# Kernel optimization log

Hardware: AMD Instinct MI355X
Metric: run time of the kernel (lower is better)

## Reference

```python
import jax, jax.numpy as jnp
import numpy as np

B, L, D_MODEL = 4, 2048, 1024
D_INNER, D_STATE, D_CONV = 2 * D_MODEL, 16, 4
DT_RANK = (D_MODEL + 15) // 16  # 64


def silu(v):
    return v * jax.nn.sigmoid(v)


def setup_inputs() -> dict:
    key = jax.random.key(0)
    ks = jax.random.split(key, 8)
    n = lambda k, shape, s: jax.random.normal(k, shape, jnp.float32) * s
    A = jnp.broadcast_to(jnp.arange(1, D_STATE + 1, dtype=jnp.float32), (D_INNER, D_STATE))
    return {
        "x": jax.random.normal(ks[0], (B, L, D_MODEL), jnp.float32),
        "in_proj_w": n(ks[1], (2 * D_INNER, D_MODEL), 0.02),
        "conv_w": n(ks[2], (D_INNER, 1, D_CONV), 0.1),
        "conv_b": jnp.zeros((D_INNER,), jnp.float32),
        "x_proj_w": n(ks[3], (DT_RANK + 2 * D_STATE, D_INNER), 0.02),
        "dt_proj_w": n(ks[4], (D_INNER, DT_RANK), 0.1),
        "dt_proj_b": n(ks[5], (D_INNER,), 0.1),
        "A_log": jnp.log(A),
        "D": jnp.ones((D_INNER,), jnp.float32),
        "out_proj_w": n(ks[6], (D_MODEL, D_INNER), 0.02),
        "ln_g": jnp.ones((D_MODEL,), jnp.float32),
        "ln_b": jnp.zeros((D_MODEL,), jnp.float32),
    }


def mamba(x, in_proj_w, conv_w, conv_b, x_proj_w, dt_proj_w, dt_proj_b, A_log, D, out_proj_w):
    # in_proj -> (B, L, 2*d_inner), split into x-branch and gate z
    xz = jnp.einsum("bld,ed->ble", x, in_proj_w)
    xm, z = jnp.split(xz, 2, axis=-1)
    # depthwise causal conv over time
    xc = jnp.swapaxes(xm, 1, 2)  # (B, d_inner, L)
    xc = jax.lax.conv_general_dilated(
        xc, conv_w, (1,), [(D_CONV - 1, 0)],
        dimension_numbers=("NCH", "OIH", "NCH"), feature_group_count=D_INNER,
    ) + conv_b[None, :, None]
    xm = silu(jnp.swapaxes(xc, 1, 2))  # (B, L, d_inner)
    # input-dependent dt, B, C
    dbc = jnp.einsum("bld,ed->ble", xm, x_proj_w)
    dt, Bm, Cm = jnp.split(dbc, [DT_RANK, DT_RANK + D_STATE], axis=-1)
    dt = jax.nn.softplus(jnp.einsum("blr,dr->bld", dt, dt_proj_w) + dt_proj_b)
    A = -jnp.exp(A_log)  # (d_inner, d_state)

    def step(h, inp):
        dt_t, B_t, C_t, x_t = inp  # (B,d_inner),(B,d_state),(B,d_state),(B,d_inner)
        h = jnp.exp(dt_t[..., None] * A) * h + (dt_t * x_t)[..., None] * B_t[:, None, :]
        y = jnp.einsum("bds,bs->bd", h, C_t)
        return h, y

    h0 = jnp.zeros((B, D_INNER, D_STATE), xm.dtype)
    xs = (jnp.swapaxes(dt, 0, 1), jnp.swapaxes(Bm, 0, 1), jnp.swapaxes(Cm, 0, 1), jnp.swapaxes(xm, 0, 1))
    _, ys = jax.lax.scan(step, h0, xs)
    y = jnp.swapaxes(ys, 0, 1) + D * xm  # (B, L, d_inner)
    y = y * silu(z)
    return jnp.einsum("bld,od->blo", y, out_proj_w)


def layer_norm(h, g, b, eps=1e-5):
    mu = jnp.mean(h, axis=-1, keepdims=True)
    var = jnp.mean(jnp.square(h - mu), axis=-1, keepdims=True)
    return (h - mu) * jax.lax.rsqrt(var + eps) * g + b


def reference(x, in_proj_w, conv_w, conv_b, x_proj_w, dt_proj_w, dt_proj_b, A_log, D, out_proj_w, ln_g, ln_b):
    y = mamba(x, in_proj_w, conv_w, conv_b, x_proj_w, dt_proj_w, dt_proj_b, A_log, D, out_proj_w)
    # dropout_level=0 (eval): identity
    return layer_norm(y + x, ln_g, ln_b)
```

## Files before the change

### kernel.cpp

```cpp
#include <hip/hip_runtime.h>
#include <hip/hip_bf16.h>

#define B_ 4
#define L_ 2048
#define DM 1024
#define DI 2048
#define DSTATE 16
#define DTR 64
#define LC 64
#define NC (L_ / LC)
#define LOG2E 1.44269504f

typedef unsigned short ushort_t;
typedef __bf16 bf16x8 __attribute__((ext_vector_type(8)));
typedef float f32x4 __attribute__((ext_vector_type(4)));
typedef float f32x16 __attribute__((ext_vector_type(16)));
typedef unsigned short u16x8 __attribute__((ext_vector_type(8)));
typedef unsigned short u16x4 __attribute__((ext_vector_type(4)));

__device__ __forceinline__ ushort_t f2bf(float f) {
    unsigned u = __builtin_bit_cast(unsigned, f);
    unsigned r = (u + 0x7FFFu + ((u >> 16) & 1u)) >> 16;
    return (ushort_t)r;
}
__device__ __forceinline__ float bf2f(ushort_t h) {
    unsigned u = ((unsigned)h) << 16;
    return __builtin_bit_cast(float, u);
}

#define CV_E0 1048576
#define CV_E1 (CV_E0 + 49152)
#define CV_E2 (CV_E1 + 32768)
#define CV_E3 (CV_E2 + 524288)
#define CV_E4 (CV_E3 + 2097152)
__global__ __launch_bounds__(256) void k_cvt5(
    const float* __restrict__ s0, ushort_t* __restrict__ d0,
    const float* __restrict__ s1, ushort_t* __restrict__ d1,
    const float* __restrict__ s2, ushort_t* __restrict__ d2,
    const float* __restrict__ s3, ushort_t* __restrict__ d3,
    const float* __restrict__ s4, ushort_t* __restrict__ d4) {
    int g = blockIdx.x * 256 + threadIdx.x;
    const float* s;
    ushort_t* dst;
    int i;
    if (g < CV_E0)      { s = s0; dst = d0; i = g * 4; }
    else if (g < CV_E1) { s = s1; dst = d1; i = (g - CV_E0) * 4; }
    else if (g < CV_E2) { s = s2; dst = d2; i = (g - CV_E1) * 4; }
    else if (g < CV_E3) { s = s3; dst = d3; i = (g - CV_E2) * 4; }
    else                { s = s4; dst = d4; i = (g - CV_E3) * 4; }
    float4 v = *reinterpret_cast<const float4*>(s + i);
    ushort4 o;
    o.x = f2bf(v.x); o.y = f2bf(v.y); o.z = f2bf(v.z); o.w = f2bf(v.w);
    *reinterpret_cast<ushort4*>(dst + i) = o;
}

#define FENCE asm volatile("" ::: "memory")
#define VM8 asm volatile("s_waitcnt vmcnt(8)" ::: "memory")
#define VM6 asm volatile("s_waitcnt vmcnt(6)" ::: "memory")
#define VM4 asm volatile("s_waitcnt vmcnt(4)" ::: "memory")
#define VM3 asm volatile("s_waitcnt vmcnt(3)" ::: "memory")
#define VM0 asm volatile("s_waitcnt vmcnt(0)" ::: "memory")

__global__ __launch_bounds__(512, 2) void k_gemm8(const ushort_t* __restrict__ Aq,
                                                  const ushort_t* __restrict__ Bq,
                                                  ushort_t* __restrict__ C) {
    __shared__ ushort_t lds[65536];
    const int tid = threadIdx.x;
    const int w = tid >> 6, lane = tid & 63;
    const int l15 = lane & 15;
    const int wm = w >> 2, wn = w & 3;
    const int bid = blockIdx.x;
    const int tm = (bid & 7) * 4 + ((bid >> 3) & 3);
    const int tn = bid >> 5;
    const int row0 = tm * 256, col0 = tn * 256;

    const int rs = w * 16 + (lane >> 2);
    const int lcs = (lane & 3) ^ ((lane >> 3) & 3);
    const int pcr = ((lane >> 4) ^ ((l15 >> 1) & 3)) * 8;
    const int aoff = wm * 4096 + l15 * 32 + pcr;
    const int boff = 8192 + (wn >> 1) * 4096 + (wn & 1) * 2048 + l15 * 32 + pcr;

    auto stg = [&](int buf, int t) {
        const ushort_t* sa = Aq + (size_t)(row0 + rs) * 1024 + t * 32 + lcs * 8;
        __builtin_amdgcn_global_load_lds(
            (const __attribute__((address_space(1))) void*)sa,
            (__attribute__((address_space(3))) void*)&lds[buf * 16384 + w * 512], 16, 0, 0);
        __builtin_amdgcn_global_load_lds(
            (const __attribute__((address_space(1))) void*)(sa + 128 * 1024),
            (__attribute__((address_space(3))) void*)&lds[buf * 16384 + 4096 + w * 512], 16, 0, 0);
        const ushort_t* sb = Bq + (size_t)(col0 + rs) * 1024 + t * 32 + lcs * 8;
        __builtin_amdgcn_global_load_lds(
            (const __attribute__((address_space(1))) void*)sb,
            (__attribute__((address_space(3))) void*)&lds[buf * 16384 + 8192 + w * 512], 16, 0, 0);
        __builtin_amdgcn_global_load_lds(
            (const __attribute__((address_space(1))) void*)(sb + 128 * 1024),
            (__attribute__((address_space(3))) void*)&lds[buf * 16384 + 12288 + w * 512], 16, 0, 0);
    };

    f32x4 acc[8][4] = {};

#define MPHASE(BUF, STAGE_STMT, WAIT_STMT)                                        \
    {                                                                             \
        bf16x8 av[8], bv[4];                                                      \
        _Pragma("unroll") for (int i_ = 0; i_ < 8; ++i_)                          \
            av[i_] = *(const bf16x8*)&lds[(BUF) * 16384 + aoff + i_ * 512];       \
        _Pragma("unroll") for (int i_ = 0; i_ < 4; ++i_)                          \
            bv[i_] = *(const bf16x8*)&lds[(BUF) * 16384 + boff + i_ * 512];       \
        STAGE_STMT;                                                               \
        FENCE; __builtin_amdgcn_s_barrier(); FENCE;                               \
        asm volatile("s_waitcnt lgkmcnt(0)" ::: "memory");                        \
        __builtin_amdgcn_sched_barrier(0);                                        \
        __builtin_amdgcn_s_setprio(1);                                            \
        _Pragma("unroll") for (int i_ = 0; i_ < 8; ++i_)                          \
            _Pragma("unroll") for (int j_ = 0; j_ < 4; ++j_)                      \
                acc[i_][j_] = __builtin_amdgcn_mfma_f32_16x16x32_bf16(            \
                    av[i_], bv[j_], acc[i_][j_], 0, 0, 0);                        \
        __builtin_amdgcn_s_setprio(0);                                            \
        WAIT_STMT;                                                                \
        FENCE; __builtin_amdgcn_s_barrier(); FENCE;                               \
    }

    stg(0, 0); stg(1, 1); stg(2, 2);
    VM8;
    FENCE; __builtin_amdgcn_s_barrier(); FENCE;

#pragma unroll 1
    for (int k = 0; k < 7; ++k) {
        const int t3 = 4 * k + 3;
        MPHASE(0, stg(3, t3), VM8);
        MPHASE(1, stg(0, t3 + 1), VM8);
        MPHASE(2, stg(1, t3 + 2), VM8);
        MPHASE(3, stg(2, t3 + 3), VM8);
    }
    MPHASE(0, stg(3, 31), VM8);
    MPHASE(1, (void)0, VM4);
    MPHASE(2, (void)0, VM0);
    MPHASE(3, (void)0, (void)0);
#undef MPHASE

#pragma unroll
    for (int mf = 0; mf < 8; ++mf)
#pragma unroll
        for (int nf = 0; nf < 4; ++nf) {
            int col = col0 + wn * 64 + nf * 16 + l15;
#pragma unroll
            for (int r = 0; r < 4; ++r) {
                int row = row0 + wm * 128 + mf * 16 + (lane >> 4) * 4 + r;
                C[(size_t)row * 4096 + col] = f2bf(acc[mf][nf][r]);
            }
        }
}

__global__ __launch_bounds__(512, 2) void k_gemm8o(const ushort_t* __restrict__ Aq,
                                                   const ushort_t* __restrict__ Bq,
                                                   ushort_t* __restrict__ C) {
    __shared__ ushort_t lds[49152];
    const int tid = threadIdx.x;
    const int w = tid >> 6, lane = tid & 63;
    const int l15 = lane & 15;
    const int wm = w >> 2, wn = w & 3;
    const int bid = blockIdx.x;
    const int tm = bid & 31, tn = bid >> 5;
    const int row0 = tm * 256, col0 = tn * 128;

    const int rs = w * 16 + (lane >> 2);
    const int lcs = (lane & 3) ^ ((lane >> 3) & 3);
    const int pcr = ((lane >> 4) ^ ((l15 >> 1) & 3)) * 8;
    const int aoff = wm * 4096 + l15 * 32 + pcr;
    const int boff = 8192 + wn * 1024 + l15 * 32 + pcr;

    auto stg = [&](int buf, int t) {
        const ushort_t* sa = Aq + (size_t)(row0 + rs) * 2048 + t * 32 + lcs * 8;
        __builtin_amdgcn_global_load_lds(
            (const __attribute__((address_space(1))) void*)sa,
            (__attribute__((address_space(3))) void*)&lds[buf * 12288 + w * 512], 16, 0, 0);
        __builtin_amdgcn_global_load_lds(
            (const __attribute__((address_space(1))) void*)(sa + 128 * 2048),
            (__attribute__((address_space(3))) void*)&lds[buf * 12288 + 4096 + w * 512], 16, 0, 0);
        const ushort_t* sb = Bq + (size_t)(col0 + rs) * 2048 + t * 32 + lcs * 8;
        __builtin_amdgcn_global_load_lds(
            (const __attribute__((address_space(1))) void*)sb,
            (__attribute__((address_space(3))) void*)&lds[buf * 12288 + 8192 + w * 512], 16, 0, 0);
    };

    f32x4 acc[8][2] = {};

#define OPHASE(BUF, STAGE_STMT, WAIT_STMT)                                        \
    {                                                                             \
        bf16x8 av[8], bv[2];                                                      \
        _Pragma("unroll") for (int i_ = 0; i_ < 8; ++i_)                          \
            av[i_] = *(const bf16x8*)&lds[(BUF) * 12288 + aoff + i_ * 512];       \
        _Pragma("unroll") for (int i_ = 0; i_ < 2; ++i_)                          \
            bv[i_] = *(const bf16x8*)&lds[(BUF) * 12288 + boff + i_ * 512];       \
        STAGE_STMT;                                                               \
        FENCE; __builtin_amdgcn_s_barrier(); FENCE;                               \
        asm volatile("s_waitcnt lgkmcnt(0)" ::: "memory");                        \
        __builtin_amdgcn_sched_barrier(0);                                        \
        __builtin_amdgcn_s_setprio(1);                                            \
        _Pragma("unroll") for (int i_ = 0; i_ < 8; ++i_)                          \
            _Pragma("unroll") for (int j_ = 0; j_ < 2; ++j_)                      \
                acc[i_][j_] = __builtin_amdgcn_mfma_f32_16x16x32_bf16(            \
                    av[i_], bv[j_], acc[i_][j_], 0, 0, 0);                        \
        __builtin_amdgcn_s_setprio(0);                                            \
        WAIT_STMT;                                                                \
        FENCE; __builtin_amdgcn_s_barrier(); FENCE;                               \
    }

    stg(0, 0); stg(1, 1); stg(2, 2);
    VM6;
    FENCE; __builtin_amdgcn_s_barrier(); FENCE;

#pragma unroll 1
    for (int k = 0; k < 15; ++k) {
        const int t3 = 4 * k + 3;
        OPHASE(0, stg(3, t3), VM6);
        OPHASE(1, stg(0, t3 + 1), VM6);
        OPHASE(2, stg(1, t3 + 2), VM6);
        OPHASE(3, stg(2, t3 + 3), VM6);
    }
    OPHASE(0, stg(3, 63), VM6);
    OPHASE(1, (void)0, VM3);
    OPHASE(2, (void)0, VM0);
    OPHASE(3, (void)0, (void)0);
#undef OPHASE

#pragma unroll
    for (int mf = 0; mf < 8; ++mf)
#pragma unroll
        for (int nf = 0; nf < 2; ++nf) {
            int col = col0 + wn * 32 + nf * 16 + l15;
#pragma unroll
            for (int r = 0; r < 4; ++r) {
                int row = row0 + wm * 128 + mf * 16 + (lane >> 4) * 4 + r;
                C[(size_t)row * 1024 + col] = f2bf(acc[mf][nf][r]);
            }
        }
}

template <int EPI, bool OUTBF>
__global__ __launch_bounds__(256) void k_gemm2(
    const ushort_t* __restrict__ A, const ushort_t* __restrict__ Bw,
    void* __restrict__ C, const float* __restrict__ bias,
    int M, int N, int K, int lda, int ldb, int ldc, int tilesM) {
    __shared__ ushort_t As[128 * 64];
    __shared__ ushort_t Bs[128 * 64];
    int tid = threadIdx.x;
    int lane = tid & 63, wv = tid >> 6;
    int wr = wv >> 1, wc = wv & 1;
    int bid = blockIdx.x;
    int tilesN = gridDim.x / tilesM;
    int per = 8 * tilesN;
    int grp = bid / per, within = bid % per;
    int tm = grp * 8 + (within & 7);
    int tn = within >> 3;
    int row0 = tm * 128, col0 = tn * 128;
    int kchunk = K / gridDim.z;
    int kbeg = blockIdx.z * kchunk, kend = kbeg + kchunk;
    float* Cf = (float*)C + (size_t)blockIdx.z * (size_t)M * ldc;

    int sr = lane >> 3;
    int sj = lane & 7;
    f32x4 acc[4][4] = {};

    for (int k0 = kbeg; k0 < kend; k0 += 64) {
        __syncthreads();
#pragma unroll
        for (int i = 0; i < 4; ++i) {
            int slot = wv * 4 + i;
            int r = slot * 8 + sr;
            int jA = sj ^ (r & 7);
            __builtin_amdgcn_global_load_lds(
                (const __attribute__((address_space(1))) void*)&A[(size_t)(row0 + r) * lda + k0 + jA * 8],
                (__attribute__((address_space(3))) void*)&As[slot * 512], 16, 0, 0);
            __builtin_amdgcn_global_load_lds(
                (const __attribute__((address_space(1))) void*)&Bw[(size_t)(col0 + r) * ldb + k0 + jA * 8],
                (__attribute__((address_space(3))) void*)&Bs[slot * 512], 16, 0, 0);
        }
        __syncthreads();
#pragma unroll
        for (int kk = 0; kk < 2; ++kk) {
            int co = kk * 32 + (lane >> 4) * 8;
            int sx = (lane & 7) << 3;
            bf16x8 af[4], bfr[4];
#pragma unroll
            for (int m = 0; m < 4; ++m) {
                int rw = wr * 64 + m * 16 + (lane & 15);
                af[m] = *reinterpret_cast<const bf16x8*>(&As[rw * 64 + (co ^ sx)]);
            }
#pragma unroll
            for (int n = 0; n < 4; ++n) {
                int rw = wc * 64 + n * 16 + (lane & 15);
                bfr[n] = *reinterpret_cast<const bf16x8*>(&Bs[rw * 64 + (co ^ sx)]);
            }
#pragma unroll
            for (int m = 0; m < 4; ++m)
#pragma unroll
                for (int n = 0; n < 4; ++n)
                    acc[m][n] = __builtin_amdgcn_mfma_f32_16x16x32_bf16(af[m], bfr[n], acc[m][n], 0, 0, 0);
        }
    }

#pragma unroll
    for (int m = 0; m < 4; ++m) {
#pragma unroll
        for (int n = 0; n < 4; ++n) {
            int col = col0 + wc * 64 + n * 16 + (lane & 15);
            if (col >= N) continue;
#pragma unroll
            for (int r = 0; r < 4; ++r) {
                int row = row0 + wr * 64 + m * 16 + (lane >> 4) * 4 + r;
                float v = acc[m][n][r];
                if (EPI == 1) {
                    v += bias[col];
                    v = (v > 20.f) ? v : log1pf(__expf(v));
                }
                if (OUTBF)
                    ((ushort_t*)C)[(size_t)row * ldc + col] = f2bf(v);
                else
                    Cf[(size_t)row * ldc + col] = v;
            }
        }
    }
}

__global__ __launch_bounds__(256) void k_red4(const float* __restrict__ p,
                                              ushort_t* __restrict__ o,
                                              int n, int stride) {
    int i = (blockIdx.x * 256 + threadIdx.x) * 4;
    if (i >= n) return;
    f32x4 a = *reinterpret_cast<const f32x4*>(&p[i]);
    f32x4 b = *reinterpret_cast<const f32x4*>(&p[i + stride]);
    f32x4 c = *reinterpret_cast<const f32x4*>(&p[i + 2 * stride]);
    f32x4 d = *reinterpret_cast<const f32x4*>(&p[i + 3 * stride]);
    ushort4 r;
    r.x = f2bf(a[0] + b[0] + c[0] + d[0]);
    r.y = f2bf(a[1] + b[1] + c[1] + d[1]);
    r.z = f2bf(a[2] + b[2] + c[2] + d[2]);
    r.w = f2bf(a[3] + b[3] + c[3] + d[3]);
    *reinterpret_cast<ushort4*>(&o[i]) = r;
}

__global__ __launch_bounds__(256) void k_conv(const ushort_t* __restrict__ xz,
                                              const float* __restrict__ w,
                                              const float* __restrict__ bias,
                                              ushort_t* __restrict__ out) {
    int d = blockIdx.x * 256 + threadIdx.x;
    int b = blockIdx.z;
    int t0 = blockIdx.y * 128;
    float w0 = w[d * 4 + 0], w1 = w[d * 4 + 1], w2 = w[d * 4 + 2], w3 = w[d * 4 + 3];
    float bi = bias[d];
    size_t base = ((size_t)b * L_) * (2 * DI) + d;
    size_t obase = ((size_t)b * L_) * DI + d;
    float x0 = (t0 >= 3) ? bf2f(xz[base + (size_t)(t0 - 3) * (2 * DI)]) : 0.f;
    float x1 = (t0 >= 2) ? bf2f(xz[base + (size_t)(t0 - 2) * (2 * DI)]) : 0.f;
    float x2 = (t0 >= 1) ? bf2f(xz[base + (size_t)(t0 - 1) * (2 * DI)]) : 0.f;
    for (int t = t0; t < t0 + 128; ++t) {
        float cur = bf2f(xz[base + (size_t)t * (2 * DI)]);
        float v = w0 * x0 + w1 * x1 + w2 * x2 + w3 * cur + bi;
        v = v / (1.f + __expf(-v));
        out[obase + (size_t)t * DI] = f2bf(v);
        x0 = x1; x1 = x2; x2 = cur;
    }
}

__global__ __launch_bounds__(256) void k_scan1(
    const ushort_t* __restrict__ dt, const ushort_t* __restrict__ xm,
    const ushort_t* __restrict__ dbc, const float* __restrict__ A_log,
    float* __restrict__ hfin, float* __restrict__ dtsum) {
    __shared__ float Bsh[LC][DSTATE];
    int tid = threadIdx.x;
    int d = blockIdx.x * 256 + tid;
    int c = blockIdx.y, b = blockIdx.z;
    f32x16 arow;
    float a1 = __expf(A_log[d * DSTATE]);
    bool ok = true;
#pragma unroll
    for (int s = 0; s < DSTATE; ++s) {
        float av = __expf(A_log[d * DSTATE + s]);
        arow[s] = -av * LOG2E;
        ok = ok && (fabsf(av - (float)(s + 1) * a1) <= 1e-4f * (float)(s + 1) * fabsf(a1) + 1e-6f);
    }
    float arow0 = -a1 * LOG2E;
    size_t rbase = (size_t)b * L_ + (size_t)c * LC;
    {
        int i = tid * 4;
        int t = i >> 4, s0 = i & 15;
        u16x4 v = *reinterpret_cast<const u16x4*>(&dbc[(rbase + t) * 96 + DTR + s0]);
#pragma unroll
        for (int j = 0; j < 4; ++j) Bsh[t][s0 + j] = bf2f(v[j]);
    }
    __syncthreads();
    f32x4 h0 = {}, h1 = {}, h2 = {}, h3 = {};
    float sd = 0.f;
    if (ok) {
        for (int t = 0; t < LC; ++t) {
            size_t ro = rbase + t;
            float dtv = bf2f(dt[ro * DI + d]);
            float xv = bf2f(xm[ro * DI + d]);
            float dx = dtv * xv;
            sd += dtv;
            float p = __builtin_amdgcn_exp2f(dtv * arow0);
            float p2 = p * p, p3 = p2 * p, p4 = p2 * p2;
            f32x4 ea = {p, p2, p3, p4};
            f32x4 eb = ea * p4, ec = eb * p4, ed = ec * p4;
            const f32x4* Bq = reinterpret_cast<const f32x4*>(&Bsh[t][0]);
            h0 = h0 * ea + Bq[0] * dx;
            h1 = h1 * eb + Bq[1] * dx;
            h2 = h2 * ec + Bq[2] * dx;
            h3 = h3 * ed + Bq[3] * dx;
        }
    } else {
        for (int t = 0; t < LC; ++t) {
            size_t ro = rbase + t;
            float dtv = bf2f(dt[ro * DI + d]);
            float xv = bf2f(xm[ro * DI + d]);
            float dx = dtv * xv;
            sd += dtv;
            const f32x4* Bq = reinterpret_cast<const f32x4*>(&Bsh[t][0]);
            f32x4 e0, e1, e2, e3;
#pragma unroll
            for (int j = 0; j < 4; ++j) {
                e0[j] = __builtin_amdgcn_exp2f(dtv * arow[j]);
                e1[j] = __builtin_amdgcn_exp2f(dtv * arow[4 + j]);
                e2[j] = __builtin_amdgcn_exp2f(dtv * arow[8 + j]);
                e3[j] = __builtin_amdgcn_exp2f(dtv * arow[12 + j]);
            }
            h0 = h0 * e0 + Bq[0] * dx;
            h1 = h1 * e1 + Bq[1] * dx;
            h2 = h2 * e2 + Bq[2] * dx;
            h3 = h3 * e3 + Bq[3] * dx;
        }
    }
    size_t hbase = (((size_t)b * NC + c) * DI + d) * DSTATE;
    *reinterpret_cast<f32x4*>(&hfin[hbase + 0]) = h0;
    *reinterpret_cast<f32x4*>(&hfin[hbase + 4]) = h1;
    *reinterpret_cast<f32x4*>(&hfin[hbase + 8]) = h2;
    *reinterpret_cast<f32x4*>(&hfin[hbase + 12]) = h3;
    dtsum[((size_t)b * NC + c) * DI + d] = sd;
}

__global__ __launch_bounds__(256) void k_scan2(
    float* __restrict__ hfin, const float* __restrict__ dtsum,
    const float* __restrict__ A_log) {
    int gid = blockIdx.x * 256 + threadIdx.x;
    int s = gid & (DSTATE - 1);
    int d = (gid >> 4) & (DI - 1);
    int b = gid >> 15;
    float Av = -__expf(A_log[d * DSTATE + s]) * LOG2E;
    float carry = 0.f;
    for (int c = 0; c < NC; ++c) {
        size_t idx = (((size_t)b * NC + c) * DI + d) * DSTATE + s;
        float loc = hfin[idx];
        hfin[idx] = carry;
        float sd = dtsum[((size_t)b * NC + c) * DI + d];
        carry = __builtin_amdgcn_exp2f(Av * sd) * carry + loc;
    }
}

__global__ __launch_bounds__(256) void k_scan3(
    const ushort_t* __restrict__ dt, const ushort_t* __restrict__ xm,
    const ushort_t* __restrict__ xz, const ushort_t* __restrict__ dbc,
    const float* __restrict__ A_log, const float* __restrict__ Dp,
    const float* __restrict__ hinit, ushort_t* __restrict__ yg) {
    __shared__ float Bsh[LC][DSTATE];
    __shared__ float Csh[LC][DSTATE];
    int tid = threadIdx.x;
    int d = blockIdx.x * 256 + tid;
    int c = blockIdx.y, b = blockIdx.z;
    f32x16 arow;
    float a1 = __expf(A_log[d * DSTATE]);
    bool ok = true;
#pragma unroll
    for (int s = 0; s < DSTATE; ++s) {
        float av = __expf(A_log[d * DSTATE + s]);
        arow[s] = -av * LOG2E;
        ok = ok && (fabsf(av - (float)(s + 1) * a1) <= 1e-4f * (float)(s + 1) * fabsf(a1) + 1e-6f);
    }
    float arow0 = -a1 * LOG2E;
    float Dd = Dp[d];
    size_t rbase = (size_t)b * L_ + (size_t)c * LC;
    {
        int e0 = tid * 8;
        int t = e0 >> 5, s0 = e0 & 31;
        u16x8 v = *reinterpret_cast<const u16x8*>(&dbc[(rbase + t) * 96 + DTR + s0]);
#pragma unroll
        for (int j = 0; j < 8; ++j) {
            int s = s0 + j;
            float f = bf2f(v[j]);
            if (s < DSTATE) Bsh[t][s] = f;
            else Csh[t][s - DSTATE] = f;
        }
    }
    __syncthreads();
    size_t hbase = (((size_t)b * NC + c) * DI + d) * DSTATE;
    f32x4 h0 = *reinterpret_cast<const f32x4*>(&hinit[hbase + 0]);
    f32x4 h1 = *reinterpret_cast<const f32x4*>(&hinit[hbase + 4]);
    f32x4 h2 = *reinterpret_cast<const f32x4*>(&hinit[hbase + 8]);
    f32x4 h3 = *reinterpret_cast<const f32x4*>(&hinit[hbase + 12]);
    if (ok) {
        for (int t = 0; t < LC; ++t) {
            size_t ro = rbase + t;
            float dtv = bf2f(dt[ro * DI + d]);
            float xv = bf2f(xm[ro * DI + d]);
            float zv = bf2f(xz[ro * (2 * DI) + DI + d]);
            float dx = dtv * xv;
            float p = __builtin_amdgcn_exp2f(dtv * arow0);
            float p2 = p * p, p3 = p2 * p, p4 = p2 * p2;
            f32x4 ea = {p, p2, p3, p4};
            f32x4 eb = ea * p4, ec = eb * p4, ed = ec * p4;
            const f32x4* Bq = reinterpret_cast<const f32x4*>(&Bsh[t][0]);
            const f32x4* Cq = reinterpret_cast<const f32x4*>(&Csh[t][0]);
            h0 = h0 * ea + Bq[0] * dx;
            h1 = h1 * eb + Bq[1] * dx;
            h2 = h2 * ec + Bq[2] * dx;
            h3 = h3 * ed + Bq[3] * dx;
            f32x4 y4 = h0 * Cq[0] + h1 * Cq[1] + h2 * Cq[2] + h3 * Cq[3];
            float y = (y4[0] + y4[1]) + (y4[2] + y4[3]) + Dd * xv;
            y *= zv / (1.f + __expf(-zv));
            yg[ro * DI + d] = f2bf(y);
        }
    } else {
        for (int t = 0; t < LC; ++t) {
            size_t ro = rbase + t;
            float dtv = bf2f(dt[ro * DI + d]);
            float xv = bf2f(xm[ro * DI + d]);
            float zv = bf2f(xz[ro * (2 * DI) + DI + d]);
            float dx = dtv * xv;
            const f32x4* Bq = reinterpret_cast<const f32x4*>(&Bsh[t][0]);
            const f32x4* Cq = reinterpret_cast<const f32x4*>(&Csh[t][0]);
            f32x4 e0, e1, e2, e3;
#pragma unroll
            for (int j = 0; j < 4; ++j) {
                e0[j] = __builtin_amdgcn_exp2f(dtv * arow[j]);
                e1[j] = __builtin_amdgcn_exp2f(dtv * arow[4 + j]);
                e2[j] = __builtin_amdgcn_exp2f(dtv * arow[8 + j]);
                e3[j] = __builtin_amdgcn_exp2f(dtv * arow[12 + j]);
            }
            h0 = h0 * e0 + Bq[0] * dx;
            h1 = h1 * e1 + Bq[1] * dx;
            h2 = h2 * e2 + Bq[2] * dx;
            h3 = h3 * e3 + Bq[3] * dx;
            f32x4 y4 = h0 * Cq[0] + h1 * Cq[1] + h2 * Cq[2] + h3 * Cq[3];
            float y = (y4[0] + y4[1]) + (y4[2] + y4[3]) + Dd * xv;
            y *= zv / (1.f + __expf(-zv));
            yg[ro * DI + d] = f2bf(y);
        }
    }
}

__global__ __launch_bounds__(256) void k_ln(const ushort_t* __restrict__ mo,
                                            const float* __restrict__ x,
                                            const float* __restrict__ g,
                                            const float* __restrict__ be,
                                            float* __restrict__ out) {
    __shared__ float red[8];
    size_t r = blockIdx.x;
    int tid = threadIdx.x;
    ushort4 mv = *reinterpret_cast<const ushort4*>(&mo[r * DM + tid * 4]);
    float4 xv = *reinterpret_cast<const float4*>(&x[r * DM + tid * 4]);
    float h0 = bf2f(mv.x) + xv.x, h1 = bf2f(mv.y) + xv.y;
    float h2 = bf2f(mv.z) + xv.z, h3 = bf2f(mv.w) + xv.w;
    float s = h0 + h1 + h2 + h3;
    float q = h0 * h0 + h1 * h1 + h2 * h2 + h3 * h3;
#pragma unroll
    for (int o = 32; o > 0; o >>= 1) {
        s += __shfl_down(s, o);
        q += __shfl_down(q, o);
    }
    int lane = tid & 63, wid = tid >> 6;
    if (lane == 0) { red[wid] = s; red[4 + wid] = q; }
    __syncthreads();
    s = red[0] + red[1] + red[2] + red[3];
    q = red[4] + red[5] + red[6] + red[7];
    float mu = s * (1.f / DM);
    float var = q * (1.f / DM) - mu * mu;
    float rs = rsqrtf(var + 1e-5f);
    float4 gv = *reinterpret_cast<const float4*>(&g[tid * 4]);
    float4 bv = *reinterpret_cast<const float4*>(&be[tid * 4]);
    float4 o;
    o.x = (h0 - mu) * rs * gv.x + bv.x;
    o.y = (h1 - mu) * rs * gv.y + bv.y;
    o.z = (h2 - mu) * rs * gv.z + bv.z;
    o.w = (h3 - mu) * rs * gv.w + bv.w;
    *reinterpret_cast<float4*>(&out[r * DM + tid * 4]) = o;
}

extern "C" void kernel_launch(void* const* d_in, const int* in_sizes, int n_in,
                              void* d_out, int out_size, void* d_ws, size_t ws_size,
                              hipStream_t stream) {
    const float* x      = (const float*)d_in[0];
    const float* w_in   = (const float*)d_in[1];
    const float* conv_w = (const float*)d_in[2];
    const float* conv_b = (const float*)d_in[3];
    const float* w_xp   = (const float*)d_in[4];
    const float* w_dt   = (const float*)d_in[5];
    const float* dt_b   = (const float*)d_in[6];
    const float* A_log  = (const float*)d_in[7];
    const float* Dp     = (const float*)d_in[8];
    const float* w_out  = (const float*)d_in[9];
    const float* ln_g   = (const float*)d_in[10];
    const float* ln_b   = (const float*)d_in[11];
    float* out = (float*)d_out;

    char* ws = (char*)d_ws;
    size_t off = 0;
    auto alloc = [&](size_t bytes) -> void* {
        void* p = ws + off;
        off += (bytes + 255) & ~(size_t)255;
        return p;
    };
    const int M = B_ * L_;
    ushort_t* w_in_b  = (ushort_t*)alloc((size_t)2 * DI * DM * 2);
    ushort_t* w_xp_b  = (ushort_t*)alloc((size_t)96 * DI * 2);
    ushort_t* w_dt_b  = (ushort_t*)alloc((size_t)DI * DTR * 2);
    ushort_t* w_out_b = (ushort_t*)alloc((size_t)DM * DI * 2);
    ushort_t* x_b     = (ushort_t*)alloc((size_t)M * DM * 2);
    ushort_t* xz      = (ushort_t*)alloc((size_t)M * 2 * DI * 2);
    ushort_t* xm      = (ushort_t*)alloc((size_t)M * DI * 2);
    ushort_t* dbc     = (ushort_t*)alloc((size_t)M * 96 * 2);
    ushort_t* dtb     = (ushort_t*)alloc((size_t)M * DI * 2);
    ushort_t* yg      = (ushort_t*)alloc((size_t)M * DI * 2);
    float*    dtsum   = (float*)alloc((size_t)B_ * NC * DI * 4);
    float*    dbc_p   = (float*)alloc((size_t)4 * M * 96 * 4);
    ushort_t* mo      = dtb;
    float*    hfin    = (float*)x_b;

    k_cvt5<<<dim3(CV_E4 / 256), 256, 0, stream>>>(
        w_in, w_in_b, w_xp, w_xp_b, w_dt, w_dt_b, w_out, w_out_b, x, x_b);

    k_gemm8<<<dim3(512), 512, 0, stream>>>(x_b, w_in_b, xz);
    k_conv<<<dim3(DI / 256, L_ / 128, B_), 256, 0, stream>>>(xz, conv_w, conv_b, xm);
    k_gemm2<0, false><<<dim3(64, 1, 4), 256, 0, stream>>>(
        xm, w_xp_b, dbc_p, nullptr, M, 96, DI, DI, DI, 96, 64);
    k_red4<<<dim3((M * 96 / 4 + 255) / 256), 256, 0, stream>>>(dbc_p, dbc, M * 96, M * 96);
    k_gemm2<1, true><<<dim3(64 * 16, 1, 1), 256, 0, stream>>>(
        dbc, w_dt_b, dtb, dt_b, M, DI, DTR, 96, DTR, DI, 64);
    k_scan1<<<dim3(DI / 256, NC, B_), 256, 0, stream>>>(dtb, xm, dbc, A_log, hfin, dtsum);
    k_scan2<<<dim3(B_ * DI * DSTATE / 256), 256, 0, stream>>>(hfin, dtsum, A_log);
    k_scan3<<<dim3(DI / 256, NC, B_), 256, 0, stream>>>(dtb, xm, xz, dbc, A_log, Dp, hfin, yg);
    k_gemm8o<<<dim3(256), 512, 0, stream>>>(yg, w_out_b, mo);
    k_ln<<<dim3(M), 256, 0, stream>>>(mo, x, ln_g, ln_b, out);
}
```

Before: 326.8 us.

## Double-buffer MFMA register fragments to overlap LDS reads with MFMA compute

Restructures the main loops of both bf16 GEMM kernels so the LDS fragment reads for the next K-tile are issued before the MFMAs on the current tile's fragments, using two register fragment sets (A/B ping-pong). It also cuts the per-phase barriers from two to one. The aim is to hide LDS read latency behind matrix-core work and reduce barrier stalls. The cost is higher VGPR pressure from the doubled fragment registers, which could hurt occupancy under launch_bounds(512,2), and it relies on the single barrier still ordering buffer reuse correctly.

```diff
diff --git a/kernel.cpp b/kernel.cpp
--- a/kernel.cpp
+++ b/kernel.cpp
@@ -60,6 +60,8 @@
 #define VM4 asm volatile("s_waitcnt vmcnt(4)" ::: "memory")
 #define VM3 asm volatile("s_waitcnt vmcnt(3)" ::: "memory")
 #define VM0 asm volatile("s_waitcnt vmcnt(0)" ::: "memory")
+#define LGKM0 do { asm volatile("s_waitcnt lgkmcnt(0)" ::: "memory"); \
+                   __builtin_amdgcn_sched_barrier(0); } while (0)
 
 __global__ __launch_bounds__(512, 2) void k_gemm8(const ushort_t* __restrict__ Aq,
                                                   const ushort_t* __restrict__ Bq,
@@ -98,45 +100,60 @@
     };
 
     f32x4 acc[8][4] = {};
-
-#define MPHASE(BUF, STAGE_STMT, WAIT_STMT)                                        \
-    {                                                                             \
-        bf16x8 av[8], bv[4];                                                      \
+    bf16x8 avA[8], bvA[4], avB[8], bvB[4];
+
+#define RD_FRAGS(BUF, AV, BV)                                                     \
+    do {                                                                          \
         _Pragma("unroll") for (int i_ = 0; i_ < 8; ++i_)                          \
-            av[i_] = *(const bf16x8*)&lds[(BUF) * 16384 + aoff + i_ * 512];       \
+            AV[i_] = *(const bf16x8*)&lds[(BUF) * 16384 + aoff + i_ * 512];       \
         _Pragma("unroll") for (int i_ = 0; i_ < 4; ++i_)                          \
-            bv[i_] = *(const bf16x8*)&lds[(BUF) * 16384 + boff + i_ * 512];       \
-        STAGE_STMT;                                                               \
-        FENCE; __builtin_amdgcn_s_barrier(); FENCE;                               \
-        asm volatile("s_waitcnt lgkmcnt(0)" ::: "memory");                        \
-        __builtin_amdgcn_sched_barrier(0);                                        \
+            BV[i_] = *(const bf16x8*)&lds[(BUF) * 16384 + boff + i_ * 512];       \
+    } while (0)
+
+#define DO_MFMA(AV, BV)                                                           \
+    do {                                                                          \
         __builtin_amdgcn_s_setprio(1);                                            \
         _Pragma("unroll") for (int i_ = 0; i_ < 8; ++i_)                          \
             _Pragma("unroll") for (int j_ = 0; j_ < 4; ++j_)                      \
                 acc[i_][j_] = __builtin_amdgcn_mfma_f32_16x16x32_bf16(            \
-                    av[i_], bv[j_], acc[i_][j_], 0, 0, 0);                        \
+                    AV[i_], BV[j_], acc[i_][j_], 0, 0, 0);                        \
         __builtin_amdgcn_s_setprio(0);                                            \
-        WAIT_STMT;                                                                \
-        FENCE; __builtin_amdgcn_s_barrier(); FENCE;                               \
-    }
+    } while (0)
 
     stg(0, 0); stg(1, 1); stg(2, 2);
     VM8;
     FENCE; __builtin_amdgcn_s_barrier(); FENCE;
+    RD_FRAGS(0, avA, bvA);
+    LGKM0;
 
 #pragma unroll 1
     for (int k = 0; k < 7; ++k) {
         const int t3 = 4 * k + 3;
-        MPHASE(0, stg(3, t3), VM8);
-        MPHASE(1, stg(0, t3 + 1), VM8);
-        MPHASE(2, stg(1, t3 + 2), VM8);
-        MPHASE(3, stg(2, t3 + 3), VM8);
-    }
-    MPHASE(0, stg(3, 31), VM8);
-    MPHASE(1, (void)0, VM4);
-    MPHASE(2, (void)0, VM0);
-    MPHASE(3, (void)0, (void)0);
-#undef MPHASE
+        stg(3, t3); VM8;
+        FENCE; __builtin_amdgcn_s_barrier(); FENCE;
+        RD_FRAGS(1, avB, bvB); DO_MFMA(avA, bvA); LGKM0;
+        stg(0, t3 + 1); VM8;
+        FENCE; __builtin_amdgcn_s_barrier(); FENCE;
+        RD_FRAGS(2, avA, bvA); DO_MFMA(avB, bvB); LGKM0;
+        stg(1, t3 + 2); VM8;
+        FENCE; __builtin_amdgcn_s_barrier(); FENCE;
+        RD_FRAGS(3, avB, bvB); DO_MFMA(avA, bvA); LGKM0;
+        stg(2, t3 + 3); VM8;
+        FENCE; __builtin_amdgcn_s_barrier(); FENCE;
+        RD_FRAGS(0, avA, bvA); DO_MFMA(avB, bvB); LGKM0;
+    }
+    stg(3, 31); VM8;
+    FENCE; __builtin_amdgcn_s_barrier(); FENCE;
+    RD_FRAGS(1, avB, bvB); DO_MFMA(avA, bvA); LGKM0;
+    VM4;
+    FENCE; __builtin_amdgcn_s_barrier(); FENCE;
+    RD_FRAGS(2, avA, bvA); DO_MFMA(avB, bvB); LGKM0;
+    VM0;
+    FENCE; __builtin_amdgcn_s_barrier(); FENCE;
+    RD_FRAGS(3, avB, bvB); DO_MFMA(avA, bvA); LGKM0;
+    DO_MFMA(avB, bvB);
+#undef RD_FRAGS
+#undef DO_MFMA
 
 #pragma unroll
     for (int mf = 0; mf < 8; ++mf)
@@ -184,45 +201,60 @@
     };
 
     f32x4 acc[8][2] = {};
-
-#define OPHASE(BUF, STAGE_STMT, WAIT_STMT)                                        \
-    {                                                                             \
-        bf16x8 av[8], bv[2];                                                      \
+    bf16x8 avA[8], bvA[2], avB[8], bvB[2];
+
+#define RD_FRAGS(BUF, AV, BV)                                                     \
+    do {                                                                          \
         _Pragma("unroll") for (int i_ = 0; i_ < 8; ++i_)                          \
-            av[i_] = *(const bf16x8*)&lds[(BUF) * 12288 + aoff + i_ * 512];       \
+            AV[i_] = *(const bf16x8*)&lds[(BUF) * 12288 + aoff + i_ * 512];       \
         _Pragma("unroll") for (int i_ = 0; i_ < 2; ++i_)                          \
-            bv[i_] = *(const bf16x8*)&lds[(BUF) * 12288 + boff + i_ * 512];       \
-        STAGE_STMT;                                                               \
-        FENCE; __builtin_amdgcn_s_barrier(); FENCE;                               \
-        asm volatile("s_waitcnt lgkmcnt(0)" ::: "memory");                        \
-        __builtin_amdgcn_sched_barrier(0);                                        \
+            BV[i_] = *(const bf16x8*)&lds[(BUF) * 12288 + boff + i_ * 512];       \
+    } while (0)
+
+#define DO_MFMA(AV, BV)                                                           \
+    do {                                                                          \
         __builtin_amdgcn_s_setprio(1);                                            \
         _Pragma("unroll") for (int i_ = 0; i_ < 8; ++i_)                          \
             _Pragma("unroll") for (int j_ = 0; j_ < 2; ++j_)                      \
                 acc[i_][j_] = __builtin_amdgcn_mfma_f32_16x16x32_bf16(            \
-                    av[i_], bv[j_], acc[i_][j_], 0, 0, 0);                        \
+                    AV[i_], BV[j_], acc[i_][j_], 0, 0, 0);                        \
         __builtin_amdgcn_s_setprio(0);                                            \
-        WAIT_STMT;                                                                \
-        FENCE; __builtin_amdgcn_s_barrier(); FENCE;                               \
-    }
+    } while (0)
 
     stg(0, 0); stg(1, 1); stg(2, 2);
     VM6;
     FENCE; __builtin_amdgcn_s_barrier(); FENCE;
+    RD_FRAGS(0, avA, bvA);
+    LGKM0;
 
 #pragma unroll 1
     for (int k = 0; k < 15; ++k) {
         const int t3 = 4 * k + 3;
-        OPHASE(0, stg(3, t3), VM6);
-        OPHASE(1, stg(0, t3 + 1), VM6);
-        OPHASE(2, stg(1, t3 + 2), VM6);
-        OPHASE(3, stg(2, t3 + 3), VM6);
-    }
-    OPHASE(0, stg(3, 63), VM6);
-    OPHASE(1, (void)0, VM3);
-    OPHASE(2, (void)0, VM0);
-    OPHASE(3, (void)0, (void)0);
-#undef OPHASE
+        stg(3, t3); VM6;
+        FENCE; __builtin_amdgcn_s_barrier(); FENCE;
+        RD_FRAGS(1, avB, bvB); DO_MFMA(avA, bvA); LGKM0;
+        stg(0, t3 + 1); VM6;
+        FENCE; __builtin_amdgcn_s_barrier(); FENCE;
+        RD_FRAGS(2, avA, bvA); DO_MFMA(avB, bvB); LGKM0;
+        stg(1, t3 + 2); VM6;
+        FENCE; __builtin_amdgcn_s_barrier(); FENCE;
+        RD_FRAGS(3, avB, bvB); DO_MFMA(avA, bvA); LGKM0;
+        stg(2, t3 + 3); VM6;
+        FENCE; __builtin_amdgcn_s_barrier(); FENCE;
+        RD_FRAGS(0, avA, bvA); DO_MFMA(avB, bvB); LGKM0;
+    }
+    stg(3, 63); VM6;
+    FENCE; __builtin_amdgcn_s_barrier(); FENCE;
+    RD_FRAGS(1, avB, bvB); DO_MFMA(avA, bvA); LGKM0;
+    VM3;
+    FENCE; __builtin_amdgcn_s_barrier(); FENCE;
+    RD_FRAGS(2, avA, bvA); DO_MFMA(avB, bvB); LGKM0;
+    VM0;
+    FENCE; __builtin_amdgcn_s_barrier(); FENCE;
+    RD_FRAGS(3, avB, bvB); DO_MFMA(avA, bvA); LGKM0;
+    DO_MFMA(avB, bvB);
+#undef RD_FRAGS
+#undef DO_MFMA
 
 #pragma unroll
     for (int mf = 0; mf < 8; ++mf)
```

After: 345.0 us. 5.6% more time.
